# Kernel tuning notes

Hardware: AMD Instinct MI355X
Metric: run time of the kernel (lower is better)

The kernel has to match this reference:

```python
import jax, jax.numpy as jnp
import numpy as np

N_EXPERTS, D_IN, D_OUT = 8, 1024, 1024
N_TOKENS = 8192


def setup_inputs() -> dict:
    key = jax.random.key(0)
    ks = jax.random.split(key, 5)
    s_in = 1.0 / np.sqrt(D_IN)
    x = jax.random.normal(ks[0], (N_TOKENS, D_IN), dtype=jnp.float32)
    W = jax.random.uniform(ks[1], (N_EXPERTS, D_IN, D_OUT), jnp.float32, -s_in, s_in)
    b = jax.random.uniform(ks[2], (N_EXPERTS, D_OUT), jnp.float32, -s_in, s_in)
    gate_W = jax.random.uniform(ks[3], (D_IN, N_EXPERTS), jnp.float32, -s_in, s_in)
    gate_b = jax.random.uniform(ks[4], (N_EXPERTS,), jnp.float32, -s_in, s_in)
    return {"x": x, "W": W, "b": b, "gate_W": gate_W, "gate_b": gate_b}


def reference(x, W, b, gate_W, gate_b):
    # gate: [n, e] softmax over experts
    gate_score = jax.nn.softmax(x @ gate_W + gate_b, axis=-1)
    # all experts applied densely: [n, e, o]
    expert_outputs = jnp.einsum('ni,eio->neo', x, W) + b[None, :, :]
    # weighted combine over expert axis: [n, o]
    return jnp.einsum('ne,neo->no', gate_score, expert_outputs)
```

## Files before the change

### kernel.cpp

```cpp
#include <hip/hip_runtime.h>
#include <hip/hip_bf16.h>
#include <cstdint>
#include <cstddef>

#define N_TOK 8192
#define D_IN  1024
#define D_OUT 1024
#define N_EXP 8
#define KTOT  (N_EXP * D_IN)

#define BM    256
#define BN    128
#define BKH   32
#define NSTEP 256

typedef __attribute__((ext_vector_type(8))) short short8;
typedef __attribute__((ext_vector_type(8))) unsigned short ushort8;
typedef __attribute__((ext_vector_type(4))) float f32x4;

__device__ __forceinline__ unsigned short f2bf(float f) {
    union { float f; unsigned int u; } v; v.f = f;
    return (unsigned short)((v.u + 0x7FFFu + ((v.u >> 16) & 1u)) >> 16);
}

__device__ __forceinline__ void load_lds16(const void* g, void* l) {
    __builtin_amdgcn_global_load_lds(
        (const __attribute__((address_space(1))) void*)g,
        (__attribute__((address_space(3))) void*)l,
        16, 0, 0);
}

__global__ __launch_bounds__(256) void prep_kernel(
    const float* __restrict__ x, const float* __restrict__ gW,
    const float* __restrict__ gbias, const float* __restrict__ W,
    unsigned short* __restrict__ xb, unsigned short* __restrict__ Wt,
    float* __restrict__ g_t) {
    const int b = blockIdx.x;
    const int t = threadIdx.x;

    if (b < 2048) {
        __shared__ float tile[64][65];
        const int e  = b >> 8;
        const int i0 = ((b >> 4) & 15) * 64;
        const int o0 = (b & 15) * 64;

        const int rr = t >> 4;
        const int rc = (t & 15) * 4;
#pragma unroll
        for (int j = 0; j < 4; ++j) {
            const float4 v = *(const float4*)(
                W + ((size_t)e * D_IN + (i0 + rr + 16 * j)) * D_OUT + o0 + rc);
            tile[rr + 16 * j][rc + 0] = v.x;
            tile[rr + 16 * j][rc + 1] = v.y;
            tile[rr + 16 * j][rc + 2] = v.z;
            tile[rr + 16 * j][rc + 3] = v.w;
        }
        __syncthreads();
        const int ow = t >> 2;
        const int c  = (t & 3) * 16;
        ushort8 v0, v1;
#pragma unroll
        for (int j = 0; j < 8; ++j) v0[j] = f2bf(tile[c + j][ow]);
#pragma unroll
        for (int j = 0; j < 8; ++j) v1[j] = f2bf(tile[c + 8 + j][ow]);
        unsigned short* dst = Wt + (size_t)(o0 + ow) * KTOT + e * D_IN + i0 + c;
        *(ushort8*)dst = v0;
        *(ushort8*)(dst + 8) = v1;
    } else {
        const int lane = t & 63;
        const int n    = (b - 2048) * 4 + (t >> 6);

        float acc[8];
#pragma unroll
        for (int e = 0; e < 8; ++e) acc[e] = 0.f;
#pragma unroll
        for (int jj = 0; jj < 4; ++jj) {
            const int i = 256 * jj + 4 * lane;
            const float4 xv = *(const float4*)(x + (size_t)n * D_IN + i);
            ushort4 u;
            u.x = f2bf(xv.x); u.y = f2bf(xv.y);
            u.z = f2bf(xv.z); u.w = f2bf(xv.w);
            *(ushort4*)(xb + (size_t)n * D_IN + i) = u;
            const float xs[4] = {xv.x, xv.y, xv.z, xv.w};
#pragma unroll
            for (int j = 0; j < 4; ++j) {
                const float* wr = gW + (size_t)(i + j) * N_EXP;
                const float4 w0 = *(const float4*)wr;
                const float4 w1 = *(const float4*)(wr + 4);
                acc[0] += xs[j] * w0.x; acc[1] += xs[j] * w0.y;
                acc[2] += xs[j] * w0.z; acc[3] += xs[j] * w0.w;
                acc[4] += xs[j] * w1.x; acc[5] += xs[j] * w1.y;
                acc[6] += xs[j] * w1.z; acc[7] += xs[j] * w1.w;
            }
        }
#pragma unroll
        for (int off = 32; off > 0; off >>= 1) {
#pragma unroll
            for (int e = 0; e < 8; ++e) acc[e] += __shfl_down(acc[e], off);
        }
        if (lane == 0) {
            float lg[8], mx = -1e30f;
#pragma unroll
            for (int e = 0; e < 8; ++e) {
                lg[e] = acc[e] + gbias[e];
                mx = fmaxf(mx, lg[e]);
            }
            float s = 0.f;
#pragma unroll
            for (int e = 0; e < 8; ++e) { lg[e] = expf(lg[e] - mx); s += lg[e]; }
            const float inv = 1.f / s;
#pragma unroll
            for (int e = 0; e < 8; ++e)
                g_t[(size_t)e * N_TOK + n] = lg[e] * inv;
        }
    }
}

__global__ __launch_bounds__(512, 1) void moe_gemm9_kernel(
    const unsigned short* __restrict__ xb,
    const unsigned short* __restrict__ Wt,
    const float* __restrict__ bias,
    const float* __restrict__ g_t,
    float* __restrict__ out) {
    __shared__ __align__(16) unsigned short A4[4][BM * BKH];
    __shared__ __align__(16) unsigned short B4[4][BN * BKH];
    __shared__ __align__(16) float g_s[N_EXP][BM];
    __shared__ __align__(16) float r_s[N_EXP][BM];
    __shared__ __align__(16) float b_s[N_EXP][BN];

    const int t    = threadIdx.x;
    const int lane = t & 63;
    const int ln15 = lane & 15;
    const int quad = lane >> 4;
    const int wave = t >> 6;
    const int wm0  = (wave >> 1) * 64;
    const int wn0  = (wave & 1) * 64;

    const int flat = blockIdx.x + 8 * blockIdx.y;
    const int bn0  = ((flat >> 3) & 7) * BN;
    const int bm0  = ((flat & 7) * 4 + (flat >> 6)) * BM;

    for (int j = t; j < N_EXP * BM; j += 512)
        g_s[j >> 8][j & 255] = g_t[(size_t)(j >> 8) * N_TOK + bm0 + (j & 255)];
    for (int j = t; j < N_EXP * BN; j += 512)
        b_s[j >> 7][j & 127] = bias[(size_t)(j >> 7) * D_OUT + bn0 + (j & 127)];
    __syncthreads();
    if (t < BM) {
        float d[N_EXP];
#pragma unroll
        for (int e = 0; e < N_EXP; ++e) d[e] = fmaxf(g_s[e][t], 1e-30f);
#pragma unroll
        for (int e = 1; e < N_EXP; ++e) r_s[e][t] = d[e - 1] / d[e];
        r_s[0][t] = d[N_EXP - 1];
    }
    __syncthreads();

    f32x4 acc[4][4];
#pragma unroll
    for (int mi = 0; mi < 4; ++mi)
#pragma unroll
        for (int ni = 0; ni < 4; ++ni)
            acc[mi][ni] = (f32x4){0.f, 0.f, 0.f, 0.f};

    const int srow = t >> 2;
    const int csw  = ((t & 3) ^ ((t >> 3) & 3)) * 8;
    const unsigned short* gA = xb + (size_t)(bm0 + srow) * D_IN + csw;
    const unsigned short* gB = Wt + (size_t)(bn0 + srow) * (size_t)KTOT + csw;
    const int wrow = wave * 16 * BKH;

    const int ksw  = (quad ^ ((ln15 >> 1) & 3)) * 8;
    const int aoff = (wm0 + ln15) * BKH + ksw;
    const int boff = (wn0 + ln15) * BKH + ksw;

#pragma unroll
    for (int s = 0; s < 3; ++s) {
        load_lds16(gA + s * BKH,              &A4[s][wrow]);
        load_lds16(gA + 128 * D_IN + s * BKH, &A4[s][128 * BKH + wrow]);
        load_lds16(gB + (size_t)s * BKH,      &B4[s][wrow]);
    }
    asm volatile("s_waitcnt vmcnt(6)" ::: "memory");
    __builtin_amdgcn_s_barrier();
    __builtin_amdgcn_sched_barrier(0);

#define HALF_STEP(h_, DO_STAGE)                                               \
  {                                                                           \
    const int slot_ = (h_) & 3;                                               \
    const unsigned short* Ab_ = &A4[slot_][0];                                \
    const unsigned short* Bb_ = &B4[slot_][0];                                \
    const int hs_ = (h_) + 3;                                                 \
    if (DO_STAGE) {                                                           \
      load_lds16(gA + ((hs_) & 31) * BKH,              &A4[(hs_) & 3][wrow]); \
      load_lds16(gA + 128 * D_IN + ((hs_) & 31) * BKH,                        \
                 &A4[(hs_) & 3][128 * BKH + wrow]);                           \
      load_lds16(gB + (size_t)(hs_) * BKH,             &B4[(hs_) & 3][wrow]); \
    }                                                                         \
    if ((h_) && !((h_) & 31)) {      \
      const int e_ = (h_) >> 5;                                               \
      _Pragma("unroll") for (int mi = 0; mi < 4; ++mi) {                      \
        const f32x4 rv = *(const f32x4*)&r_s[e_][wm0 + mi * 16 + quad * 4];   \
        _Pragma("unroll") for (int ni = 0; ni < 4; ++ni)                      \
          _Pragma("unroll") for (int r = 0; r < 4; ++r)                       \
            acc[mi][ni][r] *= rv[r];                                          \
      }                                                                       \
    }                                                                         \
    short8 af_[4], bv_[4];                                                    \
    _Pragma("unroll") for (int mi = 0; mi < 4; ++mi)                          \
      af_[mi] = *(const short8*)(Ab_ + aoff + mi * 16 * BKH);                 \
    _Pragma("unroll") for (int ni = 0; ni < 4; ++ni)                          \
      bv_[ni] = *(const short8*)(Bb_ + boff + ni * 16 * BKH);                 \
    asm volatile("s_waitcnt lgkmcnt(0)" ::: "memory");                        \
    __builtin_amdgcn_sched_barrier(0);                                        \
    __builtin_amdgcn_s_setprio(1);                                            \
    _Pragma("unroll") for (int mi = 0; mi < 4; ++mi)                          \
      _Pragma("unroll") for (int ni = 0; ni < 4; ++ni)                        \
        acc[mi][ni] = __builtin_amdgcn_mfma_f32_16x16x32_bf16(                \
            af_[mi], bv_[ni], acc[mi][ni], 0, 0, 0);                          \
    __builtin_amdgcn_s_setprio(0);                                            \
  }

#define END_WAIT(N_)                                                          \
  asm volatile("s_waitcnt vmcnt(" #N_ ")" ::: "memory");                      \
  __builtin_amdgcn_s_barrier();                                               \
  __builtin_amdgcn_sched_barrier(0);

#pragma unroll 4
    for (int h = 0; h < NSTEP - 4; ++h) {
        HALF_STEP(h, 1);
        END_WAIT(6);
    }
    HALF_STEP(252, 1);
    END_WAIT(6);
    HALF_STEP(253, 0);
    END_WAIT(3);
    HALF_STEP(254, 0);
    END_WAIT(0);
    HALF_STEP(255, 0);

#undef HALF_STEP
#undef END_WAIT

#pragma unroll
    for (int mi = 0; mi < 4; ++mi) {
        const f32x4 fin = *(const f32x4*)&r_s[0][wm0 + mi * 16 + quad * 4];
#pragma unroll
        for (int ni = 0; ni < 4; ++ni)
#pragma unroll
            for (int r = 0; r < 4; ++r) acc[mi][ni][r] *= fin[r];
    }
#pragma unroll
    for (int e = 0; e < N_EXP; ++e) {
        f32x4 gv[4];
        float bb[4];
#pragma unroll
        for (int mi = 0; mi < 4; ++mi)
            gv[mi] = *(const f32x4*)&g_s[e][wm0 + mi * 16 + quad * 4];
#pragma unroll
        for (int ni = 0; ni < 4; ++ni) bb[ni] = b_s[e][wn0 + ni * 16 + ln15];
#pragma unroll
        for (int mi = 0; mi < 4; ++mi)
#pragma unroll
            for (int ni = 0; ni < 4; ++ni)
#pragma unroll
                for (int r = 0; r < 4; ++r)
                    acc[mi][ni][r] += gv[mi][r] * bb[ni];
    }

#pragma unroll
    for (int mi = 0; mi < 4; ++mi) {
#pragma unroll
        for (int ni = 0; ni < 4; ++ni) {
            const int col  = bn0 + wn0 + ni * 16 + ln15;
            const int row0 = bm0 + wm0 + mi * 16 + quad * 4;
#pragma unroll
            for (int r = 0; r < 4; ++r)
                out[(size_t)(row0 + r) * D_OUT + col] = acc[mi][ni][r];
        }
    }
}

extern "C" void kernel_launch(void* const* d_in, const int* in_sizes, int n_in,
                              void* d_out, int out_size, void* d_ws, size_t ws_size,
                              hipStream_t stream) {
    const float* x  = (const float*)d_in[0];
    const float* W  = (const float*)d_in[1];
    const float* b  = (const float*)d_in[2];
    const float* gW = (const float*)d_in[3];
    const float* gb = (const float*)d_in[4];
    float* out = (float*)d_out;

    unsigned short* xb  = (unsigned short*)d_ws;
    unsigned short* Wt  = xb + (size_t)N_TOK * D_IN;
    float*          g_t = (float*)(Wt + (size_t)D_OUT * KTOT);

    prep_kernel<<<4096, 256, 0, stream>>>(x, gW, gb, W, xb, Wt, g_t);
    moe_gemm9_kernel<<<dim3(D_OUT / BN, N_TOK / BM), 512, 0, stream>>>(
        xb, Wt, b, g_t, out);
}
```

Measured before the change: 283.8 us.

## Double-buffer LDS fragments in registers to overlap ds_reads with MFMA

Adds two register sets of A/B fragments and, in each half-step, issues the LDS reads for the next K slice before running the MFMAs on the current one. This removes the explicit lgkmcnt(0) stall in front of each MFMA block. In exchange, the global-load wait tightens from vmcnt(6) to vmcnt(3), so global prefetch runs one stage less ahead. The change also needs extra VGPRs for the second fragment set, and the main loop is manually unrolled by two instead of using unroll 4.

```diff
diff --git a/kernel.cpp b/kernel.cpp
--- a/kernel.cpp
+++ b/kernel.cpp
@@ -116,7 +116,7 @@
     }
 }
 
-__global__ __launch_bounds__(512, 1) void moe_gemm9_kernel(
+__global__ __launch_bounds__(512, 1) void moe_gemm10_kernel(
     const unsigned short* __restrict__ xb,
     const unsigned short* __restrict__ Wt,
     const float* __restrict__ bias,
@@ -172,21 +172,26 @@
     const int aoff = (wm0 + ln15) * BKH + ksw;
     const int boff = (wn0 + ln15) * BKH + ksw;
 
+    short8 afA[4], bvA[4], afB[4], bvB[4];
+
 #pragma unroll
     for (int s = 0; s < 3; ++s) {
         load_lds16(gA + s * BKH,              &A4[s][wrow]);
         load_lds16(gA + 128 * D_IN + s * BKH, &A4[s][128 * BKH + wrow]);
         load_lds16(gB + (size_t)s * BKH,      &B4[s][wrow]);
     }
-    asm volatile("s_waitcnt vmcnt(6)" ::: "memory");
+    asm volatile("s_waitcnt vmcnt(3)" ::: "memory");
     __builtin_amdgcn_s_barrier();
     __builtin_amdgcn_sched_barrier(0);
-
-#define HALF_STEP(h_, DO_STAGE)                                               \
+#pragma unroll
+    for (int mi = 0; mi < 4; ++mi)
+        afA[mi] = *(const short8*)(&A4[0][0] + aoff + mi * 16 * BKH);
+#pragma unroll
+    for (int ni = 0; ni < 4; ++ni)
+        bvA[ni] = *(const short8*)(&B4[0][0] + boff + ni * 16 * BKH);
+
+#define HS(h_, CUR, NXT, DO_STAGE, DO_READ)                                   \
   {                                                                           \
-    const int slot_ = (h_) & 3;                                               \
-    const unsigned short* Ab_ = &A4[slot_][0];                                \
-    const unsigned short* Bb_ = &B4[slot_][0];                                \
     const int hs_ = (h_) + 3;                                                 \
     if (DO_STAGE) {                                                           \
       load_lds16(gA + ((hs_) & 31) * BKH,              &A4[(hs_) & 3][wrow]); \
@@ -194,6 +199,15 @@
                  &A4[(hs_) & 3][128 * BKH + wrow]);                           \
       load_lds16(gB + (size_t)(hs_) * BKH,             &B4[(hs_) & 3][wrow]); \
     }                                                                         \
+    if (DO_READ) {                                                            \
+      const unsigned short* An_ = &A4[((h_) + 1) & 3][0];                     \
+      const unsigned short* Bn_ = &B4[((h_) + 1) & 3][0];                     \
+      _Pragma("unroll") for (int mi = 0; mi < 4; ++mi)                        \
+        af##NXT[mi] = *(const short8*)(An_ + aoff + mi * 16 * BKH);           \
+      _Pragma("unroll") for (int ni = 0; ni < 4; ++ni)                        \
+        bv##NXT[ni] = *(const short8*)(Bn_ + boff + ni * 16 * BKH);           \
+    }                                                                         \
+    __builtin_amdgcn_sched_barrier(0);                                        \
     if ((h_) && !((h_) & 31)) {      \
       const int e_ = (h_) >> 5;                                               \
       _Pragma("unroll") for (int mi = 0; mi < 4; ++mi) {                      \
@@ -203,41 +217,34 @@
             acc[mi][ni][r] *= rv[r];                                          \
       }                                                                       \
     }                                                                         \
-    short8 af_[4], bv_[4];                                                    \
-    _Pragma("unroll") for (int mi = 0; mi < 4; ++mi)                          \
-      af_[mi] = *(const short8*)(Ab_ + aoff + mi * 16 * BKH);                 \
-    _Pragma("unroll") for (int ni = 0; ni < 4; ++ni)                          \
-      bv_[ni] = *(const short8*)(Bb_ + boff + ni * 16 * BKH);                 \
-    asm volatile("s_waitcnt lgkmcnt(0)" ::: "memory");                        \
-    __builtin_amdgcn_sched_barrier(0);                                        \
     __builtin_amdgcn_s_setprio(1);                                            \
     _Pragma("unroll") for (int mi = 0; mi < 4; ++mi)                          \
       _Pragma("unroll") for (int ni = 0; ni < 4; ++ni)                        \
         acc[mi][ni] = __builtin_amdgcn_mfma_f32_16x16x32_bf16(                \
-            af_[mi], bv_[ni], acc[mi][ni], 0, 0, 0);                          \
+            af##CUR[mi], bv##CUR[ni], acc[mi][ni], 0, 0, 0);                  \
     __builtin_amdgcn_s_setprio(0);                                            \
   }
 
-#define END_WAIT(N_)                                                          \
+#define ENDW(N_)                                                              \
   asm volatile("s_waitcnt vmcnt(" #N_ ")" ::: "memory");                      \
   __builtin_amdgcn_s_barrier();                                               \
   __builtin_amdgcn_sched_barrier(0);
 
-#pragma unroll 4
-    for (int h = 0; h < NSTEP - 4; ++h) {
-        HALF_STEP(h, 1);
-        END_WAIT(6);
-    }
-    HALF_STEP(252, 1);
-    END_WAIT(6);
-    HALF_STEP(253, 0);
-    END_WAIT(3);
-    HALF_STEP(254, 0);
-    END_WAIT(0);
-    HALF_STEP(255, 0);
-
-#undef HALF_STEP
-#undef END_WAIT
+    for (int h = 0; h < NSTEP - 4; h += 2) {
+        HS(h, A, B, 1, 1);
+        ENDW(3);
+        HS(h + 1, B, A, 1, 1);
+        ENDW(3);
+    }
+    HS(252, A, B, 1, 1);
+    ENDW(3);
+    HS(253, B, A, 0, 1);
+    ENDW(0);
+    HS(254, A, B, 0, 1);
+    HS(255, B, A, 0, 0);
+
+#undef HS
+#undef ENDW
 
 #pragma unroll
     for (int mi = 0; mi < 4; ++mi) {
@@ -293,6 +300,6 @@
     float*          g_t = (float*)(Wt + (size_t)D_OUT * KTOT);
 
     prep_kernel<<<4096, 256, 0, stream>>>(x, gW, gb, W, xb, Wt, g_t);
-    moe_gemm9_kernel<<<dim3(D_OUT / BN, N_TOK / BM), 512, 0, stream>>>(
+    moe_gemm10_kernel<<<dim3(D_OUT / BN, N_TOK / BM), 512, 0, stream>>>(
         xb, Wt, b, g_t, out);
 }
```

Measured after the change: 310.8 us. 9.5% more time.
